# Kernel optimization log

Measured on AMD Instinct MI355X. Metric: run time of the kernel, lower is better.

The kernel has to match this reference:

```python
import jax, jax.numpy as jnp
import numpy as np

BS, N, NEIGHBOR_NUM, SUPPORT = 8, 2048, 20, 7
K0, C1, C2 = 32, 64, 256  # conv_0 kernel_num, conv_1 out, conv_2 out (local_latent_size)
NUM_STRUCT = 16
LOCAL_RATE = 2048 // (8 * NUM_STRUCT)  # 16


def gather_neighbors(t, idx):
    # t: (b, v, d), idx: (b, v, n) -> (b, v, n, d)
    return jax.vmap(lambda a, i: a[i])(t, idx)


def knn_index(vertices, k):
    # (b, v, 3) -> (b, v, k) indices of k nearest neighbors (excluding self)
    inner = jnp.einsum('bid,bjd->bij', vertices, vertices)
    q = jnp.sum(vertices * vertices, axis=-1)
    dist = -2.0 * inner + q[:, :, None] + q[:, None, :]
    idx = jax.lax.top_k(-dist, k + 1)[1]  # smallest distances
    return idx[:, :, 1:]


def operator3d(neighbor_index, vertices, weights, displacement, support_num, kernel_num):
    b, v, n = neighbor_index.shape
    neigh = gather_neighbors(vertices, neighbor_index)  # (b,v,n,3)
    disp = neigh - vertices[:, :, None, :]
    theta = jax.nn.relu(disp @ displacement)            # (b,v,n,s*k)
    theta = theta.reshape(b, v, n, support_num, kernel_num)
    theta = jnp.max(theta, axis=2) * weights            # (b,v,s,k)
    return jnp.sum(theta, axis=2)                       # (b,v,k)


def operator_nd(neighbor_index, vertices, feature_map, weights, bias, displacement,
                support_num, out_channel):
    b, v, n = neighbor_index.shape
    neigh = gather_neighbors(vertices, neighbor_index)
    disp = neigh - vertices[:, :, None, :]
    theta = jax.nn.relu(disp @ displacement)            # (b,v,n,s*oc)
    feat = feature_map @ weights + bias                 # (b,v,(s+1)*oc)
    feat_center = feat[:, :, :out_channel]
    feat_support = feat[:, :, out_channel:]
    feat_support = gather_neighbors(feat_support, neighbor_index)  # (b,v,n,s*oc)
    act = (theta * feat_support).reshape(b, v, n, support_num, out_channel)
    act = jnp.sum(jnp.max(act, axis=2), axis=2)         # (b,v,oc)
    return feat_center + act


def pooling(vertices, feature_map, pooling_rate, neighbor_num, seed):
    b, v, _ = vertices.shape
    idx = knn_index(vertices, neighbor_num)
    pooled = jnp.max(gather_neighbors(feature_map, idx), axis=2)
    pool_num = v // pooling_rate
    sample_idx = np.random.default_rng(seed).permutation(v)[:pool_num]
    sample_idx = jnp.asarray(sample_idx)
    return vertices[:, sample_idx, :], pooled[:, sample_idx, :]


def setup_inputs() -> dict:
    key = jax.random.key(0)
    ks = jax.random.split(key, 9)
    vertices = jax.random.normal(ks[0], (BS, N, 3), dtype=jnp.float32)

    def unif(k, shape, stdv):
        return jax.random.uniform(k, shape, minval=-stdv, maxval=stdv, dtype=jnp.float32)

    s0 = 1.0 / np.sqrt(SUPPORT * K0)
    s1 = 1.0 / np.sqrt(C1 * (SUPPORT + 1))
    s2 = 1.0 / np.sqrt(C2 * (SUPPORT + 1))
    return {
        'vertices': vertices,
        'w0_weights': unif(ks[1], (1, 1, SUPPORT, K0), s0),
        'w0_disp': unif(ks[2], (3, SUPPORT * K0), s0),
        'w1_weights': unif(ks[3], (K0, (SUPPORT + 1) * C1), s1),
        'w1_bias': unif(ks[4], ((SUPPORT + 1) * C1,), s1),
        'w1_disp': unif(ks[5], (3, SUPPORT * C1), s1),
        'w2_weights': unif(ks[6], (C1, (SUPPORT + 1) * C2), s2),
        'w2_bias': unif(ks[7], ((SUPPORT + 1) * C2,), s2),
        'w2_disp': unif(ks[8], (3, SUPPORT * C2), s2),
    }


def reference(vertices, w0_weights, w0_disp, w1_weights, w1_bias, w1_disp,
              w2_weights, w2_bias, w2_disp):
    ni = knn_index(vertices, NEIGHBOR_NUM)
    fm0 = operator3d(ni, vertices, w0_weights, w0_disp, SUPPORT, K0)
    fm0 = jax.nn.relu(fm0)  # dropout in eval mode = identity
    fm1 = jax.nn.relu(operator_nd(ni, vertices, fm0, w1_weights, w1_bias, w1_disp, SUPPORT, C1))
    v1, fm1 = pooling(vertices, fm1, pooling_rate=8, neighbor_num=8, seed=1)
    ni2 = knn_index(v1, NEIGHBOR_NUM)
    fm2 = jax.nn.relu(operator_nd(ni2, v1, fm1, w2_weights, w2_bias, w2_disp, SUPPORT, C2))
    v2, fm3 = pooling(v1, fm2, pooling_rate=LOCAL_RATE, neighbor_num=LOCAL_RATE, seed=2)
    return v2, fm3
```

## Files before the change

### kernel.cpp

```cpp
#include <hip/hip_runtime.h>
#include <hip/hip_bf16.h>
#include <stdint.h>
#include <string.h>

#define NB   8
#define NV   2048
#define NN   20
#define SUP  7
#define K0   32
#define C1   64
#define C2   256
#define NV2  256
#define NP2  16
#define COLL_CAP 320

typedef unsigned __int128 u128;

struct CPcg { u128 state; u128 inc; bool has32; uint32_t cached; };

constexpr u128 PCG_MULT = (((u128)2549297995355413924ULL) << 64) | 4865540595714422341ULL;

constexpr uint64_t c_rotr64(uint64_t v, unsigned r) {
    return (v >> (r & 63u)) | (v << ((64u - r) & 63u));
}
constexpr uint64_t pcg_next64(CPcg& g) {
    g.state = g.state * PCG_MULT + g.inc;
    uint64_t hi = (uint64_t)(g.state >> 64);
    uint64_t lo = (uint64_t)g.state;
    return c_rotr64(hi ^ lo, (unsigned)(hi >> 58));
}
constexpr uint32_t pcg_next32(CPcg& g) {
    if (g.has32) { g.has32 = false; return g.cached; }
    uint64_t n = pcg_next64(g);
    g.has32 = true;
    g.cached = (uint32_t)(n >> 32);
    return (uint32_t)n;
}
constexpr uint64_t rand_interval(CPcg& g, uint64_t mx) {
    if (mx == 0) return 0;
    uint64_t mask = mx;
    mask |= mask >> 1; mask |= mask >> 2; mask |= mask >> 4;
    mask |= mask >> 8; mask |= mask >> 16; mask |= mask >> 32;
    uint64_t v = 0;
    while ((v = ((uint64_t)pcg_next32(g) & mask)) > mx) {
    }
    return v;
}
constexpr uint32_t hashmix(uint32_t value, uint32_t& hc) {
    value ^= hc; hc *= 0x931e8875u; value *= hc; value ^= value >> 16; return value;
}
constexpr uint32_t mixpool(uint32_t x, uint32_t y) {
    uint32_t r = (x * 0xca01f9ddu) - (y * 0x4973f715u);
    r ^= r >> 16; return r;
}
constexpr CPcg make_rng(uint32_t entropy) {
    uint32_t pool[4] = {0, 0, 0, 0};
    uint32_t hc = 0x43b0d7e5u;
    for (int i = 0; i < 4; i++) {
        uint32_t v = (i == 0) ? entropy : 0u;
        pool[i] = hashmix(v, hc);
    }
    for (int isrc = 0; isrc < 4; isrc++)
        for (int idst = 0; idst < 4; idst++)
            if (isrc != idst) pool[idst] = mixpool(pool[idst], hashmix(pool[isrc], hc));
    uint32_t w[8] = {};
    uint32_t hb = 0x8b51f9ddu;
    for (int i = 0; i < 8; i++) {
        uint32_t dv = pool[i & 3];
        dv ^= hb; hb *= 0x58f38dedu; dv *= hb; dv ^= dv >> 16; w[i] = dv;
    }
    uint64_t sd[4] = {};
    for (int k = 0; k < 4; k++) sd[k] = (uint64_t)w[2 * k] | ((uint64_t)w[2 * k + 1] << 32);
    u128 s = (((u128)sd[0]) << 64) | sd[1];
    u128 iq = (((u128)sd[2]) << 64) | sd[3];
    CPcg g{};
    g.state = 0;
    g.inc = (iq << 1) | 1;
    g.state = g.state * PCG_MULT + g.inc;
    g.state += s;
    g.state = g.state * PCG_MULT + g.inc;
    g.has32 = false; g.cached = 0;
    return g;
}

struct PermOut { int p1[256]; int p2[16]; };

constexpr PermOut compute_perms() {
    PermOut o{};
    {
        CPcg g = make_rng(1u);
        int arr[2048] = {};
        for (int i = 0; i < 2048; i++) arr[i] = i;
        for (int i = 2047; i >= 1; i--) {
            int j = (int)rand_interval(g, (uint64_t)i);
            int t = arr[i]; arr[i] = arr[j]; arr[j] = t;
        }
        for (int i = 0; i < 256; i++) o.p1[i] = arr[i];
    }
    {
        CPcg g = make_rng(2u);
        int arr[256] = {};
        for (int i = 0; i < 256; i++) arr[i] = i;
        for (int i = 255; i >= 1; i--) {
            int j = (int)rand_interval(g, (uint64_t)i);
            int t = arr[i]; arr[i] = arr[j]; arr[j] = t;
        }
        for (int i = 0; i < 16; i++) o.p2[i] = arr[i];
    }
    return o;
}

struct PermArg1 { int v[256]; };
struct PermArg2 { int v[16]; };

__global__ __launch_bounds__(384) void v2_kernel(const float* __restrict__ verts,
                                                 float* __restrict__ out,
                                                 PermArg2 cidx) {
    int t = threadIdx.x;
    if (t < NB * NP2 * 3) {
        int b = t / (NP2 * 3);
        int rem = t - b * (NP2 * 3);
        int j = rem / 3;
        int c = rem - j * 3;
        out[t] = verts[(b * NV + cidx.v[j]) * 3 + c];
    }
}

template<int N, int CPL>
__global__ __launch_bounds__(256, 4) void knn_bucket_kernel(const float* __restrict__ verts,
                                                            int* __restrict__ nbr) {
    __shared__ float sv[N * 3];
    __shared__ int hist[4][256];
    __shared__ unsigned long long coll[4][COLL_CAP];
    __shared__ int cnt[4];

    constexpr int RPB = 16;
    int bpb = N / RPB;
    int b = blockIdx.x / bpb;
    int rbase = (blockIdx.x % bpb) * RPB;

    const float* vb = verts + (size_t)b * N * 3;
    for (int t = threadIdx.x; t < N * 3; t += 256) sv[t] = vb[t];
    __syncthreads();

    int wid = threadIdx.x >> 6, lane = threadIdx.x & 63;
    int* myhist = hist[wid];
    unsigned long long* mycoll = coll[wid];

    for (int rr = 0; rr < 4; rr++) {
        int i = rbase + wid * 4 + rr;
        float vx = sv[i * 3 + 0], vy = sv[i * 3 + 1], vz = sv[i * 3 + 2];
        float qi = vx * vx + vy * vy + vz * vz;

        unsigned key[CPL];
        unsigned lmin = 0xFFFFFFFFu, lmax = 0u;
        #pragma unroll
        for (int t = 0; t < CPL; t++) {
            int j = lane + 64 * t;
            float xj = sv[j * 3 + 0], yj = sv[j * 3 + 1], zj = sv[j * 3 + 2];
            float inner = vx * xj + vy * yj + vz * zj;
            float qj = xj * xj + yj * yj + zj * zj;
            float dist = (-2.0f * inner + qi) + qj;
            unsigned u = __float_as_uint(dist);
            u = (u & 0x80000000u) ? ~u : (u | 0x80000000u);
            if (j == i) u = 0xFFFFFFFFu;
            key[t] = u;
            if (u != 0xFFFFFFFFu) {
                lmin = (u < lmin) ? u : lmin;
                lmax = (u > lmax) ? u : lmax;
            }
        }
        #pragma unroll
        for (int off = 32; off >= 1; off >>= 1) {
            unsigned o1 = (unsigned)__shfl_xor((int)lmin, off);
            unsigned o2 = (unsigned)__shfl_xor((int)lmax, off);
            lmin = (o1 < lmin) ? o1 : lmin;
            lmax = (o2 > lmax) ? o2 : lmax;
        }
        float scale = (lmax > lmin) ? 255.0f / (float)(lmax - lmin) : 0.0f;

        #pragma unroll
        for (int q = 0; q < 4; q++) myhist[lane * 4 + q] = 0;
        __asm__ volatile("s_waitcnt lgkmcnt(0)" ::: "memory");
        #pragma unroll
        for (int t = 0; t < CPL; t++) {
            int bi = (key[t] == 0xFFFFFFFFu) ? 255
                     : (int)((float)(key[t] - lmin) * scale);
            bi = (bi > 255) ? 255 : bi;
            atomicAdd(&myhist[bi], 1);
        }
        __asm__ volatile("s_waitcnt lgkmcnt(0)" ::: "memory");

        int h0 = myhist[lane * 4 + 0];
        int h1 = myhist[lane * 4 + 1];
        int h2 = myhist[lane * 4 + 2];
        int h3 = myhist[lane * 4 + 3];
        int s = h0 + h1 + h2 + h3;
        int cum = s;
        #pragma unroll
        for (int off = 1; off < 64; off <<= 1) {
            int v = __shfl_up(cum, off);
            if (lane >= off) cum += v;
        }
        unsigned long long bal = __ballot(cum >= NN);
        int L = __ffsll((long long)bal) - 1;
        int baseL = __shfl(cum, L) - __shfl(s, L);
        int g0 = __shfl(h0, L), g1 = __shfl(h1, L), g2 = __shfl(h2, L);
        int B;
        if (baseL + g0 >= NN)            B = 4 * L + 0;
        else if (baseL + g0 + g1 >= NN)  B = 4 * L + 1;
        else if (baseL + g0 + g1 + g2 >= NN) B = 4 * L + 2;
        else                              B = 4 * L + 3;

        if (lane == 0) cnt[wid] = 0;
        __asm__ volatile("s_waitcnt lgkmcnt(0)" ::: "memory");
        #pragma unroll
        for (int t = 0; t < CPL; t++) {
            int bi = (key[t] == 0xFFFFFFFFu) ? 255
                     : (int)((float)(key[t] - lmin) * scale);
            bi = (bi > 255) ? 255 : bi;
            if (bi <= B) {
                int pos = atomicAdd(&cnt[wid], 1);
                if (pos < COLL_CAP)
                    mycoll[pos] = ((unsigned long long)key[t] << 32) | (unsigned)(lane + 64 * t);
            }
        }
        __asm__ volatile("s_waitcnt lgkmcnt(0)" ::: "memory");
        int count = cnt[wid];
        if (count > COLL_CAP) count = COLL_CAP;

        int* dst = nbr + ((size_t)b * N + i) * NN;
        for (int e = lane; e < count; e += 64) {
            unsigned long long me = mycoll[e];
            int rank = 0;
            for (int m = 0; m < count; m++) rank += (mycoll[m] < me);
            if (rank < NN) dst[rank] = (int)(me & 0xFFFFFFFFull);
        }
    }
}

__global__ __launch_bounds__(256) void op3d_kernel(const float* __restrict__ verts,
                                                   const int* __restrict__ nbr,
                                                   const float* __restrict__ w0w,
                                                   const float* __restrict__ w0d,
                                                   float* __restrict__ fm0) {
    __shared__ float swd[3 * SUP * K0];
    __shared__ float sww[SUP * K0];
    for (int t = threadIdx.x; t < 3 * SUP * K0; t += 256) swd[t] = w0d[t];
    for (int t = threadIdx.x; t < SUP * K0; t += 256) sww[t] = w0w[t];
    __syncthreads();

    int gid = blockIdx.x * 256 + threadIdx.x;
    int b = gid >> 11, v = gid & (NV - 1);
    const float* vb = verts + b * NV * 3;
    float vx = vb[v * 3], vy = vb[v * 3 + 1], vz = vb[v * 3 + 2];

    const int* nb = nbr + gid * NN;
    float dx[NN], dy[NN], dz[NN];
    #pragma unroll
    for (int n = 0; n < NN; n++) {
        int j = nb[n];
        dx[n] = vb[j * 3 + 0] - vx;
        dy[n] = vb[j * 3 + 1] - vy;
        dz[n] = vb[j * 3 + 2] - vz;
    }
    float* out = fm0 + gid * K0;
    #pragma unroll 1
    for (int k = 0; k < K0; k++) {
        float acc = 0.f;
        #pragma unroll
        for (int s = 0; s < SUP; s++) {
            float w0 = swd[0 * 224 + s * K0 + k];
            float w1 = swd[1 * 224 + s * K0 + k];
            float w2 = swd[2 * 224 + s * K0 + k];
            float m = 0.f;
            #pragma unroll
            for (int n = 0; n < NN; n++) {
                float t = dx[n] * w0 + dy[n] * w1 + dz[n] * w2;
                t = fmaxf(t, 0.f);
                m = fmaxf(m, t);
            }
            acc += m * sww[s * K0 + k];
        }
        out[k] = fmaxf(acc, 0.f);
    }
}

template<int K, int N>
__global__ __launch_bounds__(256) void feat_gemm(const float* __restrict__ fm,
                                                 const float* __restrict__ w,
                                                 const float* __restrict__ bias,
                                                 float* __restrict__ feat) {
    __shared__ float sf[64][K];
    __shared__ float swt[K][64];
    int cb = blockIdx.x % (N / 64), rb = blockIdx.x / (N / 64);
    int r0 = rb * 64, c0 = cb * 64;

    for (int t = threadIdx.x; t < 64 * K; t += 256)
        sf[t / K][t % K] = fm[(size_t)(r0 + t / K) * K + (t % K)];
    for (int t = threadIdx.x; t < K * 64; t += 256)
        swt[t >> 6][t & 63] = w[(size_t)(t >> 6) * N + c0 + (t & 63)];
    __syncthreads();

    int col = threadIdx.x & 63, rg = threadIdx.x >> 6;
    float bv = bias[c0 + col];
    float acc[16];
    #pragma unroll
    for (int r = 0; r < 16; r++) acc[r] = bv;
    #pragma unroll 1
    for (int k = 0; k < K; k++) {
        float wk = swt[k][col];
        #pragma unroll
        for (int r = 0; r < 16; r++) acc[r] += sf[rg * 16 + r][k] * wk;
    }
    #pragma unroll
    for (int r = 0; r < 16; r++)
        feat[(size_t)(r0 + rg * 16 + r) * N + c0 + col] = acc[r];
}

__global__ __launch_bounds__(256) void opnd1_gather(const float* __restrict__ verts,
                                                    const int* __restrict__ nbr,
                                                    const float* __restrict__ feat1,
                                                    const float* __restrict__ w1d,
                                                    float* __restrict__ fm1) {
    __shared__ float swd[3 * SUP * C1];
    for (int t = threadIdx.x; t < 3 * SUP * C1; t += 256) swd[t] = w1d[t];
    __syncthreads();

    int wid = threadIdx.x >> 6, lane = threadIdx.x & 63;
    int vtx = blockIdx.x * 4 + wid;
    int b = vtx >> 11, v = vtx & (NV - 1);
    const float* vb = verts + b * NV * 3;
    const int* nb = nbr + vtx * NN;
    float vx = vb[v * 3], vy = vb[v * 3 + 1], vz = vb[v * 3 + 2];

    float w0r[SUP], w1r[SUP], w2r[SUP];
    #pragma unroll
    for (int ss = 0; ss < SUP; ss++) {
        w0r[ss] = swd[0 * (SUP * C1) + ss * C1 + lane];
        w1r[ss] = swd[1 * (SUP * C1) + ss * C1 + lane];
        w2r[ss] = swd[2 * (SUP * C1) + ss * C1 + lane];
    }

    const float* fb = feat1 + (size_t)b * NV * (8 * C1);
    float m[SUP];
    #pragma unroll
    for (int ss = 0; ss < SUP; ss++) m[ss] = -3.4e38f;

    #pragma unroll 4
    for (int n = 0; n < NN; n++) {
        int j = nb[n];
        float dx = vb[j * 3 + 0] - vx;
        float dy = vb[j * 3 + 1] - vy;
        float dz = vb[j * 3 + 2] - vz;
        const float* row = fb + (size_t)j * (8 * C1) + C1 + lane;
        #pragma unroll
        for (int ss = 0; ss < SUP; ss++) {
            float th = fmaxf(dx * w0r[ss] + dy * w1r[ss] + dz * w2r[ss], 0.f);
            m[ss] = fmaxf(m[ss], th * row[ss * C1]);
        }
    }
    float fcen = fb[(size_t)v * (8 * C1) + lane];
    float total = 0.f;
    #pragma unroll
    for (int ss = 0; ss < SUP; ss++) total += m[ss];
    fm1[vtx * C1 + lane] = fmaxf(fcen + total, 0.f);
}

__global__ __launch_bounds__(256) void opnd2_gather(const float* __restrict__ v1,
                                                    const int* __restrict__ nbr2,
                                                    const float* __restrict__ feat2,
                                                    const float* __restrict__ w2d,
                                                    float* __restrict__ fm2) {
    __shared__ float swd[3 * SUP * C2];
    for (int t = threadIdx.x; t < 3 * SUP * C2; t += 256) swd[t] = w2d[t];
    __syncthreads();

    int jj = threadIdx.x >> 6, lane = threadIdx.x & 63;
    int vtx = blockIdx.x;
    int b = vtx >> 8, v = vtx & (NV2 - 1);
    const float* vb = v1 + b * NV2 * 3;
    const int* nb = nbr2 + vtx * NN;
    float vx = vb[v * 3], vy = vb[v * 3 + 1], vz = vb[v * 3 + 2];

    int cj = jj * 64 + lane;
    float w0r[SUP], w1r[SUP], w2r[SUP];
    #pragma unroll
    for (int ss = 0; ss < SUP; ss++) {
        w0r[ss] = swd[0 * (SUP * C2) + ss * C2 + cj];
        w1r[ss] = swd[1 * (SUP * C2) + ss * C2 + cj];
        w2r[ss] = swd[2 * (SUP * C2) + ss * C2 + cj];
    }
    const float* fb = feat2 + (size_t)b * NV2 * (8 * C2);

    float m[SUP];
    #pragma unroll
    for (int ss = 0; ss < SUP; ss++) m[ss] = -3.4e38f;

    #pragma unroll 4
    for (int n = 0; n < NN; n++) {
        int j = nb[n];
        float dx = vb[j * 3 + 0] - vx;
        float dy = vb[j * 3 + 1] - vy;
        float dz = vb[j * 3 + 2] - vz;
        const float* row = fb + (size_t)j * (8 * C2) + C2 + cj;
        #pragma unroll
        for (int ss = 0; ss < SUP; ss++) {
            float th = fmaxf(dx * w0r[ss] + dy * w1r[ss] + dz * w2r[ss], 0.f);
            m[ss] = fmaxf(m[ss], th * row[ss * C2]);
        }
    }
    float total = 0.f;
    #pragma unroll
    for (int ss = 0; ss < SUP; ss++) total += m[ss];
    float fcen = fb[(size_t)v * (8 * C2) + cj];
    fm2[(size_t)vtx * C2 + cj] = fmaxf(fcen + total, 0.f);
}

__global__ __launch_bounds__(256) void pool1_kernel(const float* __restrict__ verts,
                                                    const int* __restrict__ nbr1,
                                                    const float* __restrict__ fm1,
                                                    float* __restrict__ v1,
                                                    float* __restrict__ fm1p,
                                                    PermArg1 pa) {
    int wid = threadIdx.x >> 6, lane = threadIdx.x & 63;
    int gid = blockIdx.x * 4 + wid;
    int b = gid >> 8, p = gid & 255;
    int sv = pa.v[p];
    const int* nb = nbr1 + (b * NV + sv) * NN;
    float m = -3.4e38f;
    #pragma unroll
    for (int n = 0; n < 8; n++) {
        m = fmaxf(m, fm1[(b * NV + nb[n]) * C1 + lane]);
    }
    fm1p[gid * C1 + lane] = m;
    if (lane < 3) v1[gid * 3 + lane] = verts[(b * NV + sv) * 3 + lane];
}

__global__ __launch_bounds__(256) void pool2_kernel(const int* __restrict__ nbr2,
                                                    const float* __restrict__ fm2,
                                                    float* __restrict__ out,
                                                    PermArg2 pa) {
    int wid = threadIdx.x >> 6, lane = threadIdx.x & 63;
    int gid = blockIdx.x * 4 + wid;
    int b = gid >> 4, p = gid & 15;
    int sv = pa.v[p];
    const int* nb = nbr2 + (b * NV2 + sv) * NN;
    #pragma unroll 1
    for (int jj = 0; jj < 4; jj++) {
        int c = lane + jj * 64;
        float m = -3.4e38f;
        #pragma unroll
        for (int n = 0; n < 16; n++) {
            m = fmaxf(m, fm2[(b * NV2 + nb[n]) * C2 + c]);
        }
        out[NB * NP2 * 3 + gid * C2 + c] = m;
    }
}

extern "C" void kernel_launch(void* const* d_in, const int* in_sizes, int n_in,
                              void* d_out, int out_size, void* d_ws, size_t ws_size,
                              hipStream_t stream) {
    (void)in_sizes; (void)n_in; (void)out_size; (void)ws_size;
    const float* verts = (const float*)d_in[0];
    const float* w0w = (const float*)d_in[1];
    const float* w0d = (const float*)d_in[2];
    const float* w1w = (const float*)d_in[3];
    const float* w1b = (const float*)d_in[4];
    const float* w1d = (const float*)d_in[5];
    const float* w2w = (const float*)d_in[6];
    const float* w2b = (const float*)d_in[7];
    const float* w2d = (const float*)d_in[8];
    float* out = (float*)d_out;

    static const PermOut perms = compute_perms();

    PermArg1 pa1;
    PermArg2 pa2, pac;
    memcpy(pa1.v, perms.p1, sizeof(pa1.v));
    memcpy(pa2.v, perms.p2, sizeof(pa2.v));
    for (int j = 0; j < 16; j++) pac.v[j] = perms.p1[perms.p2[j]];

    char* ws = (char*)d_ws;
    size_t off = 0;
    auto alloc = [&](size_t bytes) -> void* {
        void* p = ws + off;
        off += (bytes + 255) & ~(size_t)255;
        return p;
    };
    int*   nbr1  = (int*)  alloc((size_t)NB * NV * NN * 4);
    float* fm0   = (float*)alloc((size_t)NB * NV * K0 * 4);
    float* feat1 = (float*)alloc((size_t)NB * NV * 8 * C1 * 4);
    float* fm1   = (float*)alloc((size_t)NB * NV * C1 * 4);
    float* v1    = (float*)alloc((size_t)NB * NV2 * 3 * 4);
    float* fm1p  = (float*)alloc((size_t)NB * NV2 * C1 * 4);
    int*   nbr2  = (int*)  alloc((size_t)NB * NV2 * NN * 4);
    float* feat2 = (float*)alloc((size_t)NB * NV2 * 8 * C2 * 4);
    float* fm2   = (float*)alloc((size_t)NB * NV2 * C2 * 4);

    v2_kernel<<<1, 384, 0, stream>>>(verts, out, pac);
    knn_bucket_kernel<NV, NV / 64><<<NB * (NV / 16), 256, 0, stream>>>(verts, nbr1);
    op3d_kernel<<<64, 256, 0, stream>>>(verts, nbr1, w0w, w0d, fm0);
    feat_gemm<K0, 8 * C1><<<(NB * NV / 64) * (8 * C1 / 64), 256, 0, stream>>>(fm0, w1w, w1b, feat1);
    opnd1_gather<<<NB * NV / 4, 256, 0, stream>>>(verts, nbr1, feat1, w1d, fm1);
    pool1_kernel<<<NB * NV2 / 4, 256, 0, stream>>>(verts, nbr1, fm1, v1, fm1p, pa1);
    knn_bucket_kernel<NV2, NV2 / 64><<<NB * (NV2 / 16), 256, 0, stream>>>(v1, nbr2);
    feat_gemm<C1, 8 * C2><<<(NB * NV2 / 64) * (8 * C2 / 64), 256, 0, stream>>>(fm1p, w2w, w2b, feat2);
    opnd2_gather<<<NB * NV2, 256, 0, stream>>>(v1, nbr2, feat2, w2d, fm2);
    pool2_kernel<<<32, 256, 0, stream>>>(nbr2, fm2, out, pa2);
}
```

Baseline: 247.9 us.

## Pack vertices to float4 and read KNN candidates from global memory instead of LDS

Adds a pack kernel, plus a store in pool1, that write vertices as padded float4. The KNN kernel then drops its per-block shared-memory copy of all vertices and loads candidates directly from global or L2 with a single 16-byte load. It also halves rows per block, doubling the block count, and raises the occupancy hint to 8. The aim is to remove the redundant full-cloud LDS staging in every block and to improve occupancy. The cost is an extra kernel launch and more L2 traffic for candidate reads.

```diff
diff --git a/kernel.cpp b/kernel.cpp
--- a/kernel.cpp
+++ b/kernel.cpp
@@ -126,30 +126,35 @@
     }
 }
 
+__global__ __launch_bounds__(256) void pack_kernel(const float* __restrict__ verts,
+                                                   float4* __restrict__ vq) {
+    int gid = blockIdx.x * 256 + threadIdx.x;
+    vq[gid] = make_float4(verts[gid * 3 + 0], verts[gid * 3 + 1],
+                          verts[gid * 3 + 2], 0.f);
+}
+
 template<int N, int CPL>
-__global__ __launch_bounds__(256, 4) void knn_bucket_kernel(const float* __restrict__ verts,
+__global__ __launch_bounds__(256, 8) void knn_bucket_kernel(const float4* __restrict__ vq,
                                                             int* __restrict__ nbr) {
-    __shared__ float sv[N * 3];
     __shared__ int hist[4][256];
     __shared__ unsigned long long coll[4][COLL_CAP];
     __shared__ int cnt[4];
 
-    constexpr int RPB = 16;
+    constexpr int RPB = 8;
     int bpb = N / RPB;
     int b = blockIdx.x / bpb;
     int rbase = (blockIdx.x % bpb) * RPB;
 
-    const float* vb = verts + (size_t)b * N * 3;
-    for (int t = threadIdx.x; t < N * 3; t += 256) sv[t] = vb[t];
-    __syncthreads();
+    const float4* vb = vq + (size_t)b * N;
 
     int wid = threadIdx.x >> 6, lane = threadIdx.x & 63;
     int* myhist = hist[wid];
     unsigned long long* mycoll = coll[wid];
 
-    for (int rr = 0; rr < 4; rr++) {
-        int i = rbase + wid * 4 + rr;
-        float vx = sv[i * 3 + 0], vy = sv[i * 3 + 1], vz = sv[i * 3 + 2];
+    for (int rr = 0; rr < 2; rr++) {
+        int i = rbase + wid * 2 + rr;
+        float4 vi = vb[i];
+        float vx = vi.x, vy = vi.y, vz = vi.z;
         float qi = vx * vx + vy * vy + vz * vz;
 
         unsigned key[CPL];
@@ -157,7 +162,8 @@
         #pragma unroll
         for (int t = 0; t < CPL; t++) {
             int j = lane + 64 * t;
-            float xj = sv[j * 3 + 0], yj = sv[j * 3 + 1], zj = sv[j * 3 + 2];
+            float4 vj = vb[j];
+            float xj = vj.x, yj = vj.y, zj = vj.z;
             float inner = vx * xj + vy * yj + vz * zj;
             float qj = xj * xj + yj * yj + zj * zj;
             float dist = (-2.0f * inner + qi) + qj;
@@ -421,6 +427,7 @@
                                                     const int* __restrict__ nbr1,
                                                     const float* __restrict__ fm1,
                                                     float* __restrict__ v1,
+                                                    float4* __restrict__ v1q,
                                                     float* __restrict__ fm1p,
                                                     PermArg1 pa) {
     int wid = threadIdx.x >> 6, lane = threadIdx.x & 63;
@@ -435,6 +442,10 @@
     }
     fm1p[gid * C1 + lane] = m;
     if (lane < 3) v1[gid * 3 + lane] = verts[(b * NV + sv) * 3 + lane];
+    if (lane == 0) {
+        const float* src = verts + (size_t)(b * NV + sv) * 3;
+        v1q[gid] = make_float4(src[0], src[1], src[2], 0.f);
+    }
 }
 
 __global__ __launch_bounds__(256) void pool2_kernel(const int* __restrict__ nbr2,
@@ -488,23 +499,26 @@
         off += (bytes + 255) & ~(size_t)255;
         return p;
     };
-    int*   nbr1  = (int*)  alloc((size_t)NB * NV * NN * 4);
-    float* fm0   = (float*)alloc((size_t)NB * NV * K0 * 4);
-    float* feat1 = (float*)alloc((size_t)NB * NV * 8 * C1 * 4);
-    float* fm1   = (float*)alloc((size_t)NB * NV * C1 * 4);
-    float* v1    = (float*)alloc((size_t)NB * NV2 * 3 * 4);
-    float* fm1p  = (float*)alloc((size_t)NB * NV2 * C1 * 4);
-    int*   nbr2  = (int*)  alloc((size_t)NB * NV2 * NN * 4);
-    float* feat2 = (float*)alloc((size_t)NB * NV2 * 8 * C2 * 4);
-    float* fm2   = (float*)alloc((size_t)NB * NV2 * C2 * 4);
+    int*    nbr1  = (int*)   alloc((size_t)NB * NV * NN * 4);
+    float*  fm0   = (float*) alloc((size_t)NB * NV * K0 * 4);
+    float*  feat1 = (float*) alloc((size_t)NB * NV * 8 * C1 * 4);
+    float*  fm1   = (float*) alloc((size_t)NB * NV * C1 * 4);
+    float*  v1    = (float*) alloc((size_t)NB * NV2 * 3 * 4);
+    float*  fm1p  = (float*) alloc((size_t)NB * NV2 * C1 * 4);
+    int*    nbr2  = (int*)   alloc((size_t)NB * NV2 * NN * 4);
+    float*  feat2 = (float*) alloc((size_t)NB * NV2 * 8 * C2 * 4);
+    float*  fm2   = (float*) alloc((size_t)NB * NV2 * C2 * 4);
+    float4* vq    = (float4*)alloc((size_t)NB * NV * 16);
+    float4* v1q   = (float4*)alloc((size_t)NB * NV2 * 16);
 
     v2_kernel<<<1, 384, 0, stream>>>(verts, out, pac);
-    knn_bucket_kernel<NV, NV / 64><<<NB * (NV / 16), 256, 0, stream>>>(verts, nbr1);
+    pack_kernel<<<NB * NV / 256, 256, 0, stream>>>(verts, vq);
+    knn_bucket_kernel<NV, NV / 64><<<NB * (NV / 8), 256, 0, stream>>>(vq, nbr1);
     op3d_kernel<<<64, 256, 0, stream>>>(verts, nbr1, w0w, w0d, fm0);
     feat_gemm<K0, 8 * C1><<<(NB * NV / 64) * (8 * C1 / 64), 256, 0, stream>>>(fm0, w1w, w1b, feat1);
     opnd1_gather<<<NB * NV / 4, 256, 0, stream>>>(verts, nbr1, feat1, w1d, fm1);
-    pool1_kernel<<<NB * NV2 / 4, 256, 0, stream>>>(verts, nbr1, fm1, v1, fm1p, pa1);
-    knn_bucket_kernel<NV2, NV2 / 64><<<NB * (NV2 / 16), 256, 0, stream>>>(v1, nbr2);
+    pool1_kernel<<<NB * NV2 / 4, 256, 0, stream>>>(verts, nbr1, fm1, v1, v1q, fm1p, pa1);
+    knn_bucket_kernel<NV2, NV2 / 64><<<NB * (NV2 / 8), 256, 0, stream>>>(v1q, nbr2);
     feat_gemm<C1, 8 * C2><<<(NB * NV2 / 64) * (8 * C2 / 64), 256, 0, stream>>>(fm1p, w2w, w2b, feat2);
     opnd2_gather<<<NB * NV2, 256, 0, stream>>>(v1, nbr2, feat2, w2d, fm2);
     pool2_kernel<<<32, 256, 0, stream>>>(nbr2, fm2, out, pa2);
```

Measured after the change: 652.5 us. 163% more time.
